# Optimization experiments

Measured on AMD Instinct MI355X. Metric: run time of the kernel, lower is better.

Reference implementation:

```python
import jax, jax.numpy as jnp
import numpy as np

BATCH, L = 32, 32
DATA_SIZE = 8
XDIM = DATA_SIZE + 1        # xs feature dim (9)
IN_DIM = DATA_SIZE + 2      # 1 (time) + XDIM = 10
WIDTH, DEPTH = 32, 5


def _layer_shapes():
    shapes = [(WIDTH, IN_DIM), (WIDTH,)]
    for _ in range(DEPTH - 1):
        shapes += [(WIDTH, WIDTH), (WIDTH,)]
    shapes += [(1, WIDTH), (1,)]
    return shapes

_SHAPES = _layer_shapes()
D_THETA = int(sum(int(np.prod(s)) for s in _SHAPES))  # 4609


def _unravel(theta):
    # theta: (..., D_THETA) -> list of (W, b) pairs, vectorized over leading dims
    flats, off = [], 0
    for s in _SHAPES:
        n = int(np.prod(s))
        flats.append(theta[..., off:off + n].reshape(theta.shape[:-1] + s))
        off += n
    return list(zip(flats[0::2], flats[1::2]))


def _root_mlp(params, x):
    # x: (..., IN_DIM); each (W, b) carries matching leading dims (hypernetwork)
    h = x
    for W, b in params[:-1]:
        h = jax.nn.relu(jnp.einsum('...oi,...i->...o', W, h) + b)
    W, b = params[-1]
    return jnp.einsum('...oi,...i->...o', W, h) + b


def setup_inputs() -> dict:
    key = jax.random.key(0)
    k_x, k_t, k_A, k_B, k_th = jax.random.split(key, 5)
    xs = jax.random.normal(k_x, (BATCH, L, XDIM), dtype=jnp.float32)
    ts = jnp.sort(jax.random.uniform(k_t, (BATCH, L, 1), dtype=jnp.float32), axis=1)
    # 'trained'-style params: A near identity for a stable linear recurrence
    A = jnp.eye(D_THETA, dtype=jnp.float32) \
        + 0.01 * jax.random.normal(k_A, (D_THETA, D_THETA), dtype=jnp.float32) / np.sqrt(D_THETA)
    B = 0.02 * jax.random.normal(k_B, (D_THETA, IN_DIM), dtype=jnp.float32)
    theta_0 = 0.1 * jax.random.normal(k_th, (D_THETA,), dtype=jnp.float32)
    return {"xs": xs, "ts": ts, "A": A, "B": B, "theta_0": theta_0}


def reference(xs, ts, A, B, theta_0):
    # u_t = concat([t_t, x_t]); scan input delta du_t = u_t - u_{t-1}, du_0 = 0
    u = jnp.concatenate([ts, xs], axis=-1)              # (B, L, IN_DIM)
    du = jnp.diff(u, axis=1, prepend=u[:, :1])          # (B, L, IN_DIM)

    def step(theta, du_t):                               # theta: (B, D_THETA)
        theta_next = theta @ A.T + du_t @ B.T
        return theta_next, theta_next

    theta_init = jnp.broadcast_to(theta_0, (xs.shape[0], D_THETA))
    _, theta_outs = jax.lax.scan(step, theta_init, jnp.swapaxes(du, 0, 1))
    theta_outs = jnp.swapaxes(theta_outs, 0, 1)          # (B, L, D_THETA)

    params = _unravel(theta_outs)
    ys_hat = _root_mlp(params, u)                        # (B, L, 1)
    return ys_hat
```

## Files before the change

### kernel.cpp

```cpp
#include <hip/hip_runtime.h>

typedef __attribute__((ext_vector_type(8))) short bfrag8;
typedef __attribute__((ext_vector_type(4))) float f32x4;

#define N_TH   4609
#define NIB    289
#define NKC    152
#define TSTR   4612
#define NB     32
#define NL     32

#define OF_PROW  0
#define OF_PMF   55488
#define OF_PCOLB 429248
#define OF_PMCH  577216
#define OF_PMCL  1317056
#define OF_CFH   2056896
#define OF_CFL   2220736
#define OF_A2M   2384576

__device__ __forceinline__ unsigned short f2bf(float v) {
    unsigned int u = __float_as_uint(v);
    return (unsigned short)((u + 0x7fffu + ((u >> 16) & 1u)) >> 16);
}
__device__ __forceinline__ float bf2f(unsigned short h) {
    return __uint_as_float((unsigned int)h << 16);
}

__global__ __launch_bounds__(256) void k_p0(const float* __restrict__ th0,
                                            const float* __restrict__ Bm,
                                            float* __restrict__ Prow,
                                            unsigned short* __restrict__ Pmf,
                                            unsigned short* __restrict__ PmcH,
                                            unsigned short* __restrict__ PmcL) {
    int idx = blockIdx.x * 256 + threadIdx.x;
    if (idx >= NKC * 32 * 16) return;
    int i = idx >> 4, c = idx & 15;
    float v = 0.f;
    if (i < N_TH && c < 11) {
        if (c == 0) v = th0[i];
        else v = Bm[(size_t)i * 10 + (c - 1)];
    }
    if (i < 4624 && c < 12) Prow[i * 12 + c] = v;
    int ch = i >> 5, kr = i & 31;
    size_t slot = (size_t)ch * 512 + (size_t)(((kr >> 3) * 16 + c) << 3) + (kr & 7);
    Pmf[slot] = (v == 0.f) ? (unsigned short)0 : f2bf(v);
    Pmf[(size_t)NKC * 512 + slot] = 0;
    if (c >= 1 && c <= 10 && i < N_TH) {
        int kidx = c - 1;
        size_t s2 = ((size_t)(i >> 4) << 9) +
                    (size_t)((((kidx & 31) >> 3) * 16 + (i & 15)) << 3) + (kidx & 7);
        unsigned short h = f2bf(v);
        PmcH[s2] = h;
        PmcL[s2] = f2bf(v - bf2f(h));
    }
}

__global__ __launch_bounds__(256) void k_cf(const float* __restrict__ xs,
                                            const float* __restrict__ ts,
                                            unsigned short* __restrict__ CfH,
                                            unsigned short* __restrict__ CfL) {
    int idx = blockIdx.x * 256 + threadIdx.x;
    if (idx >= 10 * 64 * 512) return;
    int kk = idx & 7;
    int l  = (idx >> 3) & 63;
    int mt = (idx >> 9) & 63;
    int kc = idx >> 15;
    int bt = mt * 16 + (l & 15);
    int t = bt & 31, b = bt >> 5;
    int kidx = kc * 32 + (l >> 4) * 8 + kk;
    int j = kidx / 10, d = kidx - j * 10;
    float v = 0.f;
    if (j < t) {
        int tt = t - j;
        v = (d == 0) ? (ts[b * NL + tt] - ts[b * NL + tt - 1])
                     : (xs[(size_t)(b * NL + tt) * 9 + d - 1] -
                        xs[(size_t)(b * NL + tt - 1) * 9 + d - 1]);
    }
    unsigned short h = f2bf(v);
    CfH[idx] = h;
    CfL[idx] = f2bf(v - bf2f(h));
}

__global__ __launch_bounds__(256) void k_tr(const float* __restrict__ A,
                                            unsigned short* __restrict__ A2m) {
    const int tid = threadIdx.x;
    const int lane = tid & 63, w = tid >> 6;
    const int task = blockIdx.x * 4 + w;
    const int ib = task / NKC, m = task - ib * NKC;
    const int r = lane & 15, g = lane >> 4;
    const int row = ib * 16 + r;
    const int c0 = m * 32 + g * 8;

    float f[8];
    if (row < N_TH && c0 + 7 < N_TH) {
        const float* ap = A + (size_t)row * N_TH + c0;
#pragma unroll
        for (int e = 0; e < 8; e++) f[e] = ap[e];
    } else {
#pragma unroll
        for (int e = 0; e < 8; e++) {
            int c = c0 + e;
            f[e] = (row < N_TH && c < N_TH) ? A[(size_t)row * N_TH + c] : 0.f;
        }
    }
#pragma unroll
    for (int e = 0; e < 8; e++)
        if (row == c0 + e) f[e] -= 1.f;

    uint4 o;
    o.x = (unsigned int)f2bf(f[0]) | ((unsigned int)f2bf(f[1]) << 16);
    o.y = (unsigned int)f2bf(f[2]) | ((unsigned int)f2bf(f[3]) << 16);
    o.z = (unsigned int)f2bf(f[4]) | ((unsigned int)f2bf(f[5]) << 16);
    o.w = (unsigned int)f2bf(f[6]) | ((unsigned int)f2bf(f[7]) << 16);
    ((uint4*)A2m)[(size_t)task * 64 + lane] = o;
}

__global__ __launch_bounds__(512, 2) void k_step4(const bfrag8* __restrict__ A2m,
                                                  const bfrag8* __restrict__ Bsrc,
                                                  unsigned short* __restrict__ Pdst,
                                                  float* __restrict__ Prow,
                                                  float* __restrict__ PcolB,
                                                  unsigned short* __restrict__ PmcH,
                                                  unsigned short* __restrict__ PmcL,
                                                  int k) {
    __shared__ float red[8][256];
    const int tid = threadIdx.x, lane = tid & 63, w = tid >> 6;
    const int ib = blockIdx.x;
    const int cs = w * 19;
    const bfrag8* ap = A2m + ((size_t)ib * NKC + cs) * 64 + lane;
    const bfrag8* bp = Bsrc + (size_t)cs * 64 + lane;

    bfrag8 a[19], b[19];
#pragma unroll
    for (int c = 0; c < 19; c++) a[c] = ap[(size_t)c * 64];
#pragma unroll
    for (int c = 0; c < 19; c++) b[c] = bp[(size_t)c * 64];

    f32x4 acc = {0.f, 0.f, 0.f, 0.f};
#pragma unroll
    for (int c = 0; c < 19; c++)
        acc = __builtin_amdgcn_mfma_f32_16x16x32_bf16(a[c], b[c], acc, 0, 0, 0);

#pragma unroll
    for (int r = 0; r < 4; r++)
        red[w][(((lane >> 4) * 4) + r) * 16 + (lane & 15)] = acc[r];
    __syncthreads();

    if (tid < 256) {
        const int row = tid >> 4, c = tid & 15;
        const int i = ib * 16 + row;
        if (i < N_TH && c < 11) {
            float s = red[0][tid] + red[1][tid] + red[2][tid] + red[3][tid]
                    + red[4][tid] + red[5][tid] + red[6][tid] + red[7][tid];
            float pnew = Prow[i * 12 + c] + s;
            Prow[i * 12 + c] = pnew;
            if (c == 0) {
                PcolB[(size_t)(k - 1) * 4624 + i] = pnew;
            } else if (k <= 31) {
                int kidx = k * 10 + (c - 1);
                int kc = kidx >> 5, kr = kidx & 31;
                size_t slot = ((size_t)(kc * NIB + (i >> 4)) << 9) +
                              (size_t)(((kr >> 3) * 16 + (i & 15)) << 3) + (kr & 7);
                unsigned short h = f2bf(pnew);
                PmcH[slot] = h;
                PmcL[slot] = f2bf(pnew - bf2f(h));
            }
            if (k <= 31) {
                int ch2 = i >> 5, kr2 = i & 31;
                Pdst[(size_t)ch2 * 512 +
                     (size_t)(((kr2 >> 3) * 16 + c) << 3) + (kr2 & 7)] = f2bf(pnew);
            }
        }
    }
}

__global__ __launch_bounds__(256) void k_conv(const bfrag8* __restrict__ CfH,
                                              const bfrag8* __restrict__ CfL,
                                              const bfrag8* __restrict__ PmcH,
                                              const bfrag8* __restrict__ PmcL,
                                              const float* __restrict__ PcolB,
                                              float* __restrict__ theta) {
    const int tid = threadIdx.x, lane = tid & 63, w = tid >> 6;
    const int icg = blockIdx.x;
    const int mt  = blockIdx.y * 4 + w;
    const int icmax = NIB - icg * 8;

    f32x4 acc[8];
#pragma unroll
    for (int t8 = 0; t8 < 8; t8++) acc[t8] = (f32x4){0.f, 0.f, 0.f, 0.f};

#pragma unroll 1
    for (int kc = 0; kc < 10; kc++) {
        bfrag8 ah = CfH[(size_t)(kc * 64 + mt) * 64 + lane];
        bfrag8 al = CfL[(size_t)(kc * 64 + mt) * 64 + lane];
#pragma unroll
        for (int t8 = 0; t8 < 8; t8++) {
            if (t8 < icmax) {
                size_t bo = (size_t)(kc * NIB + icg * 8 + t8) * 64 + lane;
                bfrag8 bh = PmcH[bo];
                bfrag8 bl = PmcL[bo];
                acc[t8] = __builtin_amdgcn_mfma_f32_16x16x32_bf16(ah, bh, acc[t8], 0, 0, 0);
                acc[t8] = __builtin_amdgcn_mfma_f32_16x16x32_bf16(ah, bl, acc[t8], 0, 0, 0);
                acc[t8] = __builtin_amdgcn_mfma_f32_16x16x32_bf16(al, bh, acc[t8], 0, 0, 0);
            }
        }
    }

    const int n = lane & 15, gg = lane >> 4;
#pragma unroll
    for (int t8 = 0; t8 < 8; t8++) {
        if (t8 < icmax) {
            int i = (icg * 8 + t8) * 16 + n;
            if (i < N_TH) {
#pragma unroll
                for (int r = 0; r < 4; r++) {
                    int bt = mt * 16 + gg * 4 + r;
                    int t = bt & 31;
                    theta[(size_t)bt * TSTR + i] = acc[t8][r] + PcolB[(size_t)t * 4624 + i];
                }
            }
        }
    }
}

__global__ __launch_bounds__(256) void k_mlp(const float* __restrict__ xs,
                                             const float* __restrict__ ts,
                                             const float* __restrict__ theta,
                                             float* __restrict__ out) {
    const int tid  = threadIdx.x;
    const int lane = tid & 63;
    const int half = (lane >> 5) & 1;
    const int o    = lane & 31;
    const int wv   = tid >> 6;
    const int bt   = blockIdx.x * 8 + wv * 2 + half;
    const int b = bt >> 5, t = bt & 31;
    const float* th = theta + (size_t)bt * TSTR;

    float u[10];
    u[0] = ts[b * NL + t];
#pragma unroll
    for (int d = 0; d < 9; d++) u[1 + d] = xs[(b * NL + t) * 9 + d];

    float acc = th[320 + o];
#pragma unroll
    for (int i = 0; i < 10; i++) acc = fmaf(th[o * 10 + i], u[i], acc);
    float h = fmaxf(acc, 0.f);

#pragma unroll
    for (int l = 0; l < 4; l++) {
        int base = 352 + l * 1056;
        float a2 = th[base + 1024 + o];
#pragma unroll
        for (int i = 0; i < 32; i++)
            a2 = fmaf(th[base + o * 32 + i], __shfl(h, i, 32), a2);
        h = fmaxf(a2, 0.f);
    }

    float contrib = th[4576 + o] * h;
#pragma unroll
    for (int m = 16; m >= 1; m >>= 1) contrib += __shfl_xor(contrib, m, 32);
    if (o == 0) out[bt] = contrib + th[4608];
}

extern "C" void kernel_launch(void* const* d_in, const int* in_sizes, int n_in,
                              void* d_out, int out_size, void* d_ws, size_t ws_size,
                              hipStream_t stream) {
    const float* xs  = (const float*)d_in[0];
    const float* ts  = (const float*)d_in[1];
    const float* A   = (const float*)d_in[2];
    const float* Bm  = (const float*)d_in[3];
    const float* th0 = (const float*)d_in[4];
    float* out = (float*)d_out;
    float* ws  = (float*)d_ws;

    float*          Prow  = ws + OF_PROW;
    unsigned short* Pmf   = (unsigned short*)(ws + OF_PMF);
    float*          PcolB = ws + OF_PCOLB;
    unsigned short* PmcH  = (unsigned short*)(ws + OF_PMCH);
    unsigned short* PmcL  = (unsigned short*)(ws + OF_PMCL);
    unsigned short* CfH   = (unsigned short*)(ws + OF_CFH);
    unsigned short* CfL   = (unsigned short*)(ws + OF_CFL);
    unsigned short* A2m   = (unsigned short*)(ws + OF_A2M);
    float*          theta = ws + OF_A2M;

    k_p0<<<304, 256, 0, stream>>>(th0, Bm, Prow, Pmf, PmcH, PmcL);
    k_cf<<<1280, 256, 0, stream>>>(xs, ts, CfH, CfL);
    k_tr<<<10982, 256, 0, stream>>>(A, A2m);

    for (int k = 1; k <= 32; k++) {
        const unsigned short* src = Pmf + (size_t)((k - 1) & 1) * (NKC * 512);
        unsigned short* dst       = Pmf + (size_t)(k & 1) * (NKC * 512);
        k_step4<<<NIB, 512, 0, stream>>>((const bfrag8*)A2m, (const bfrag8*)src,
                                         dst, Prow, PcolB, PmcH, PmcL, k);
    }

    k_conv<<<dim3(37, 16), 256, 0, stream>>>((const bfrag8*)CfH, (const bfrag8*)CfL,
                                             (const bfrag8*)PmcH, (const bfrag8*)PmcL,
                                             PcolB, theta);
    k_mlp<<<128, 256, 0, stream>>>(xs, ts, theta, out);
}
```

Measured before the change: 423.3 us.

## Split per-step matvec into split-K partial kernel plus finalize kernel

Each recurrence step was one kernel of 289 blocks of 512 threads, every wave doing 19 MFMAs over a K-slice. It becomes two kernels. A split-K kernel launches a 145x8 grid of 256-thread blocks, each wave doing about 10 MFMAs and writing partial sums to a workspace buffer. A second kernel sums the 8 partials and does the state update and scatter. The goal is more parallelism and occupancy across CUs to hide load latency, at the cost of twice as many launches per step (64 extra) and a round trip of partials through global memory.

```diff
diff --git a/kernel.cpp b/kernel.cpp
--- a/kernel.cpp
+++ b/kernel.cpp
@@ -18,6 +18,7 @@
 #define OF_CFH   2056896
 #define OF_CFL   2220736
 #define OF_A2M   2384576
+#define OF_PART  13630144
 
 __device__ __forceinline__ unsigned short f2bf(float v) {
     unsigned int u = __float_as_uint(v);
@@ -116,62 +117,81 @@
     ((uint4*)A2m)[(size_t)task * 64 + lane] = o;
 }
 
-__global__ __launch_bounds__(512, 2) void k_step4(const bfrag8* __restrict__ A2m,
+__global__ __launch_bounds__(256, 4) void k_stepP(const bfrag8* __restrict__ A2m,
                                                   const bfrag8* __restrict__ Bsrc,
-                                                  unsigned short* __restrict__ Pdst,
-                                                  float* __restrict__ Prow,
-                                                  float* __restrict__ PcolB,
-                                                  unsigned short* __restrict__ PmcH,
-                                                  unsigned short* __restrict__ PmcL,
-                                                  int k) {
-    __shared__ float red[8][256];
+                                                  float* __restrict__ part) {
+    __shared__ float red[4][256];
     const int tid = threadIdx.x, lane = tid & 63, w = tid >> 6;
-    const int ib = blockIdx.x;
-    const int cs = w * 19;
-    const bfrag8* ap = A2m + ((size_t)ib * NKC + cs) * 64 + lane;
-    const bfrag8* bp = Bsrc + (size_t)cs * 64 + lane;
-
-    bfrag8 a[19], b[19];
-#pragma unroll
-    for (int c = 0; c < 19; c++) a[c] = ap[(size_t)c * 64];
-#pragma unroll
-    for (int c = 0; c < 19; c++) b[c] = bp[(size_t)c * 64];
+    const int g = blockIdx.x;
+    const int ks = blockIdx.y;
+    const int ibv = 2 * g + (w >> 1);
+    const int ib = (ibv < NIB) ? ibv : (NIB - 1);
+    const int half = w & 1;
+    const int cbase = ks * 19 + half * 10;
+    const int cnt = half ? 9 : 10;
+
+    const bfrag8* ap = A2m + ((size_t)ib * NKC + cbase) * 64 + lane;
+    const bfrag8* bp = Bsrc + (size_t)cbase * 64 + lane;
+
+    bfrag8 a[10], b[10];
+#pragma unroll
+    for (int c = 0; c < 10; c++) {
+        int cc = (c < cnt) ? c : cnt - 1;
+        a[c] = ap[(size_t)cc * 64];
+        b[c] = bp[(size_t)cc * 64];
+    }
+    __builtin_amdgcn_sched_barrier(0);
 
     f32x4 acc = {0.f, 0.f, 0.f, 0.f};
 #pragma unroll
-    for (int c = 0; c < 19; c++)
-        acc = __builtin_amdgcn_mfma_f32_16x16x32_bf16(a[c], b[c], acc, 0, 0, 0);
+    for (int c = 0; c < 10; c++)
+        if (c < cnt)
+            acc = __builtin_amdgcn_mfma_f32_16x16x32_bf16(a[c], b[c], acc, 0, 0, 0);
 
 #pragma unroll
     for (int r = 0; r < 4; r++)
         red[w][(((lane >> 4) * 4) + r) * 16 + (lane & 15)] = acc[r];
     __syncthreads();
 
-    if (tid < 256) {
-        const int row = tid >> 4, c = tid & 15;
-        const int i = ib * 16 + row;
-        if (i < N_TH && c < 11) {
-            float s = red[0][tid] + red[1][tid] + red[2][tid] + red[3][tid]
-                    + red[4][tid] + red[5][tid] + red[6][tid] + red[7][tid];
-            float pnew = Prow[i * 12 + c] + s;
-            Prow[i * 12 + c] = pnew;
-            if (c == 0) {
-                PcolB[(size_t)(k - 1) * 4624 + i] = pnew;
-            } else if (k <= 31) {
-                int kidx = k * 10 + (c - 1);
-                int kc = kidx >> 5, kr = kidx & 31;
-                size_t slot = ((size_t)(kc * NIB + (i >> 4)) << 9) +
-                              (size_t)(((kr >> 3) * 16 + (i & 15)) << 3) + (kr & 7);
-                unsigned short h = f2bf(pnew);
-                PmcH[slot] = h;
-                PmcL[slot] = f2bf(pnew - bf2f(h));
-            }
-            if (k <= 31) {
-                int ch2 = i >> 5, kr2 = i & 31;
-                Pdst[(size_t)ch2 * 512 +
-                     (size_t)(((kr2 >> 3) * 16 + c) << 3) + (kr2 & 7)] = f2bf(pnew);
-            }
-        }
+    float s_lo = red[0][tid] + red[1][tid];
+    float s_hi = red[2][tid] + red[3][tid];
+    part[((size_t)ks * 290 + 2 * g) * 256 + tid]     = s_lo;
+    part[((size_t)ks * 290 + 2 * g + 1) * 256 + tid] = s_hi;
+}
+
+__global__ __launch_bounds__(256) void k_finP(const float* __restrict__ part,
+                                              float* __restrict__ Prow,
+                                              float* __restrict__ PcolB,
+                                              unsigned short* __restrict__ PmcH,
+                                              unsigned short* __restrict__ PmcL,
+                                              unsigned short* __restrict__ Pdst,
+                                              int k) {
+    const int tid = threadIdx.x;
+    const int ib = blockIdx.x;
+    const int row = tid >> 4, c = tid & 15;
+    const int i = ib * 16 + row;
+    if (i >= N_TH || c >= 11) return;
+    float s = 0.f;
+#pragma unroll
+    for (int ks = 0; ks < 8; ks++)
+        s += part[((size_t)ks * 290 + ib) * 256 + tid];
+    float pnew = Prow[i * 12 + c] + s;
+    Prow[i * 12 + c] = pnew;
+    if (c == 0) {
+        PcolB[(size_t)(k - 1) * 4624 + i] = pnew;
+    } else if (k <= 31) {
+        int kidx = k * 10 + (c - 1);
+        int kc = kidx >> 5, kr = kidx & 31;
+        size_t slot = ((size_t)(kc * NIB + (i >> 4)) << 9) +
+                      (size_t)(((kr >> 3) * 16 + (i & 15)) << 3) + (kr & 7);
+        unsigned short h = f2bf(pnew);
+        PmcH[slot] = h;
+        PmcL[slot] = f2bf(pnew - bf2f(h));
+    }
+    if (k <= 31) {
+        int ch2 = i >> 5, kr2 = i & 31;
+        Pdst[(size_t)ch2 * 512 +
+             (size_t)(((kr2 >> 3) * 16 + c) << 3) + (kr2 & 7)] = f2bf(pnew);
     }
 }
 
@@ -282,6 +302,7 @@
     unsigned short* CfH   = (unsigned short*)(ws + OF_CFH);
     unsigned short* CfL   = (unsigned short*)(ws + OF_CFL);
     unsigned short* A2m   = (unsigned short*)(ws + OF_A2M);
+    float*          part  = ws + OF_PART;
     float*          theta = ws + OF_A2M;
 
     k_p0<<<304, 256, 0, stream>>>(th0, Bm, Prow, Pmf, PmcH, PmcL);
@@ -291,8 +312,9 @@
     for (int k = 1; k <= 32; k++) {
         const unsigned short* src = Pmf + (size_t)((k - 1) & 1) * (NKC * 512);
         unsigned short* dst       = Pmf + (size_t)(k & 1) * (NKC * 512);
-        k_step4<<<NIB, 512, 0, stream>>>((const bfrag8*)A2m, (const bfrag8*)src,
-                                         dst, Prow, PcolB, PmcH, PmcL, k);
+        k_stepP<<<dim3(145, 8), 256, 0, stream>>>((const bfrag8*)A2m,
+                                                  (const bfrag8*)src, part);
+        k_finP<<<NIB, 256, 0, stream>>>(part, Prow, PcolB, PmcH, PmcL, dst, k);
     }
 
     k_conv<<<dim3(37, 16), 256, 0, stream>>>((const bfrag8*)CfH, (const bfrag8*)CfL,
```

Measured after the change: 436.3 us. +3.1%, slower.

## Fuse 32 scan step launches into one persistent cooperative kernel with grid sync

Applied to the files above, without the earlier changes.

Replaces 32 separate k_step4 launches with a single cooperative kernel of 256 blocks that loops over the time steps and uses grid.sync between them. The A matrix fragments stay in registers across all steps, and each block handles one or two row tiles so that 289 tiles fit in 256 blocks. The running P value is kept in a register instead of being reloaded from global memory. This is meant to remove per-step launch overhead and repeated A reloads, at the cost of grid-wide barriers, higher register pressure from two A fragment sets, and an uneven load across blocks.

```diff
diff --git a/kernel.cpp b/kernel.cpp
--- a/kernel.cpp
+++ b/kernel.cpp
@@ -1,4 +1,7 @@
 #include <hip/hip_runtime.h>
+#include <hip/hip_cooperative_groups.h>
+
+namespace cg = cooperative_groups;
 
 typedef __attribute__((ext_vector_type(8))) short bfrag8;
 typedef __attribute__((ext_vector_type(4))) float f32x4;
@@ -116,62 +119,94 @@
     ((uint4*)A2m)[(size_t)task * 64 + lane] = o;
 }
 
-__global__ __launch_bounds__(512, 2) void k_step4(const bfrag8* __restrict__ A2m,
-                                                  const bfrag8* __restrict__ Bsrc,
-                                                  unsigned short* __restrict__ Pdst,
-                                                  float* __restrict__ Prow,
-                                                  float* __restrict__ PcolB,
-                                                  unsigned short* __restrict__ PmcH,
-                                                  unsigned short* __restrict__ PmcL,
-                                                  int k) {
-    __shared__ float red[8][256];
+__global__ __launch_bounds__(512, 2) void k_scan(const bfrag8* __restrict__ A2m,
+                                                 unsigned short* __restrict__ Pmf,
+                                                 const float* __restrict__ Prow0,
+                                                 float* __restrict__ PcolB,
+                                                 unsigned short* __restrict__ PmcH,
+                                                 unsigned short* __restrict__ PmcL) {
+    cg::grid_group grid = cg::this_grid();
+    __shared__ float redA[8][256];
+    __shared__ float redB[8][256];
     const int tid = threadIdx.x, lane = tid & 63, w = tid >> 6;
-    const int ib = blockIdx.x;
+    const int bid = blockIdx.x;
+    const int ib1 = bid;
+    const bool heavy = (bid < NIB - 256);
+    const int ib2 = 256 + bid;
     const int cs = w * 19;
-    const bfrag8* ap = A2m + ((size_t)ib * NKC + cs) * 64 + lane;
-    const bfrag8* bp = Bsrc + (size_t)cs * 64 + lane;
-
-    bfrag8 a[19], b[19];
-#pragma unroll
-    for (int c = 0; c < 19; c++) a[c] = ap[(size_t)c * 64];
-#pragma unroll
-    for (int c = 0; c < 19; c++) b[c] = bp[(size_t)c * 64];
-
-    f32x4 acc = {0.f, 0.f, 0.f, 0.f};
-#pragma unroll
-    for (int c = 0; c < 19; c++)
-        acc = __builtin_amdgcn_mfma_f32_16x16x32_bf16(a[c], b[c], acc, 0, 0, 0);
-
-#pragma unroll
-    for (int r = 0; r < 4; r++)
-        red[w][(((lane >> 4) * 4) + r) * 16 + (lane & 15)] = acc[r];
-    __syncthreads();
-
-    if (tid < 256) {
-        const int row = tid >> 4, c = tid & 15;
-        const int i = ib * 16 + row;
-        if (i < N_TH && c < 11) {
-            float s = red[0][tid] + red[1][tid] + red[2][tid] + red[3][tid]
-                    + red[4][tid] + red[5][tid] + red[6][tid] + red[7][tid];
-            float pnew = Prow[i * 12 + c] + s;
-            Prow[i * 12 + c] = pnew;
-            if (c == 0) {
-                PcolB[(size_t)(k - 1) * 4624 + i] = pnew;
+
+    bfrag8 a1[19], a2[19];
+    {
+        const bfrag8* ap1 = A2m + ((size_t)ib1 * NKC + cs) * 64 + lane;
+#pragma unroll
+        for (int c = 0; c < 19; c++) a1[c] = ap1[(size_t)c * 64];
+        const bfrag8* ap2 = A2m + ((size_t)(heavy ? ib2 : ib1) * NKC + cs) * 64 + lane;
+#pragma unroll
+        for (int c = 0; c < 19; c++) a2[c] = ap2[(size_t)c * 64];
+    }
+
+    const int et = tid & 255;
+    const int erow = et >> 4, ec = et & 15;
+    const int eib = (tid < 256) ? ib1 : ib2;
+    const int ei = eib * 16 + erow;
+    const bool evalid = (ei < N_TH) && (ec < 11) && (tid < 256 || heavy);
+    float pval = evalid ? Prow0[ei * 12 + ec] : 0.f;
+
+    for (int k = 1; k <= 32; k++) {
+        const bfrag8* bp = (const bfrag8*)(Pmf + (size_t)((k - 1) & 1) * (NKC * 512))
+                           + (size_t)cs * 64 + lane;
+        unsigned short* Pdst = Pmf + (size_t)(k & 1) * (NKC * 512);
+
+        f32x4 acc1 = {0.f, 0.f, 0.f, 0.f};
+        f32x4 acc2 = {0.f, 0.f, 0.f, 0.f};
+        bfrag8 rb[4];
+#pragma unroll
+        for (int c = 0; c < 4; c++) rb[c] = bp[(size_t)c * 64];
+#pragma unroll
+        for (int c = 0; c < 19; c++) {
+            bfrag8 bc = rb[c & 3];
+            if (c + 4 < 19) rb[c & 3] = bp[(size_t)(c + 4) * 64];
+            acc1 = __builtin_amdgcn_mfma_f32_16x16x32_bf16(a1[c], bc, acc1, 0, 0, 0);
+            acc2 = __builtin_amdgcn_mfma_f32_16x16x32_bf16(a2[c], bc, acc2, 0, 0, 0);
+        }
+
+#pragma unroll
+        for (int r = 0; r < 4; r++) {
+            int off = (((lane >> 4) * 4) + r) * 16 + (lane & 15);
+            redA[w][off] = acc1[r];
+            redB[w][off] = acc2[r];
+        }
+        __syncthreads();
+
+        if (evalid) {
+            float s = 0.f;
+            if (tid < 256) {
+#pragma unroll
+                for (int ww = 0; ww < 8; ww++) s += redA[ww][et];
+            } else {
+#pragma unroll
+                for (int ww = 0; ww < 8; ww++) s += redB[ww][et];
+            }
+            pval += s;
+            if (ec == 0) {
+                PcolB[(size_t)(k - 1) * 4624 + ei] = pval;
             } else if (k <= 31) {
-                int kidx = k * 10 + (c - 1);
+                int kidx = k * 10 + (ec - 1);
                 int kc = kidx >> 5, kr = kidx & 31;
-                size_t slot = ((size_t)(kc * NIB + (i >> 4)) << 9) +
-                              (size_t)(((kr >> 3) * 16 + (i & 15)) << 3) + (kr & 7);
-                unsigned short h = f2bf(pnew);
+                size_t slot = ((size_t)(kc * NIB + (ei >> 4)) << 9) +
+                              (size_t)(((kr >> 3) * 16 + (ei & 15)) << 3) + (kr & 7);
+                unsigned short h = f2bf(pval);
                 PmcH[slot] = h;
-                PmcL[slot] = f2bf(pnew - bf2f(h));
+                PmcL[slot] = f2bf(pval - bf2f(h));
             }
             if (k <= 31) {
-                int ch2 = i >> 5, kr2 = i & 31;
+                int ch2 = ei >> 5, kr2 = ei & 31;
                 Pdst[(size_t)ch2 * 512 +
-                     (size_t)(((kr2 >> 3) * 16 + c) << 3) + (kr2 & 7)] = f2bf(pnew);
-            }
-        }
+                     (size_t)(((kr2 >> 3) * 16 + ec) << 3) + (kr2 & 7)] = f2bf(pval);
+            }
+        }
+        __syncthreads();
+        grid.sync();
     }
 }
 
@@ -288,11 +323,18 @@
     k_cf<<<1280, 256, 0, stream>>>(xs, ts, CfH, CfL);
     k_tr<<<10982, 256, 0, stream>>>(A, A2m);
 
-    for (int k = 1; k <= 32; k++) {
-        const unsigned short* src = Pmf + (size_t)((k - 1) & 1) * (NKC * 512);
-        unsigned short* dst       = Pmf + (size_t)(k & 1) * (NKC * 512);
-        k_step4<<<NIB, 512, 0, stream>>>((const bfrag8*)A2m, (const bfrag8*)src,
-                                         dst, Prow, PcolB, PmcH, PmcL, k);
+    {
+        const bfrag8* A2m_c = (const bfrag8*)A2m;
+        const float*  Prow_c = Prow;
+        void* args[6];
+        args[0] = (void*)&A2m_c;
+        args[1] = (void*)&Pmf;
+        args[2] = (void*)&Prow_c;
+        args[3] = (void*)&PcolB;
+        args[4] = (void*)&PmcH;
+        args[5] = (void*)&PmcL;
+        hipLaunchCooperativeKernel((const void*)k_scan, dim3(256), dim3(512),
+                                   args, 0, stream);
     }
 
     k_conv<<<dim3(37, 16), 256, 0, stream>>>((const bfrag8*)CfH, (const bfrag8*)CfL,
```

Measured after the change: 1.111 ms. +162.4%, slower.
